# Optimization experiments

Measured on AMD Instinct MI355X. Metric: run time of the kernel, lower is better.

## Reference

```python
import jax, jax.numpy as jnp
import numpy as np

D = 2048   # input_dim == output_dim (original scatter-adds into zeros_like(x))
E = 16     # num_experts
K = 2      # expert_top_k
B = 2048   # tokens


def setup_inputs() -> dict:
    key = jax.random.key(0)
    ks = jax.random.split(key, 6)
    s = 0.02
    return {
        "x":  jax.random.normal(ks[0], (B, D), jnp.float32),
        "W1": (jax.random.normal(ks[1], (E, D, D), jnp.float32) * s),
        "b1": jnp.zeros((E, D), jnp.float32),
        "W2": (jax.random.normal(ks[2], (E, D, D), jnp.float32) * s),
        "b2": jnp.zeros((E, D), jnp.float32),
        "Wg": (jax.random.normal(ks[3], (D, E), jnp.float32) * s),
        "bg": jnp.zeros((E,), jnp.float32),
    }


def reference(x, W1, b1, W2, b2, Wg, bg):
    # --- gating ---
    gate_scores = x @ Wg + bg                                  # (B, E)
    topk_scores, topk_idx = jax.lax.top_k(gate_scores, K)      # (B, K)
    gate_act = jax.nn.softmax(topk_scores, axis=-1)            # (B, K) softmax over top-k only
    onehot = jax.nn.one_hot(topk_idx, E, dtype=x.dtype)        # (B, K, E)
    combine = jnp.einsum('bk,bke->be', gate_act, onehot)       # (B, E) gate weight per expert (0 if unrouted)
    routing_mask = onehot.sum(axis=1)                          # (B, E) in {0,1}

    # --- expert MLPs (dense grouped form; unrouted tokens zeroed by combine) ---
    h = jax.nn.relu(jnp.einsum('bd,edh->ebh', x, W1) + b1[:, None, :])   # (E, B, D)
    y = jnp.einsum('ebh,eho->ebo', h, W2) + b2[:, None, :]               # (E, B, D)
    out = jnp.einsum('ebo,be->bo', y, combine)                           # (B, D) weighted scatter-add combine

    # --- aux losses (torch.var is unbiased, ddof=1) ---
    loads = routing_mask.sum(axis=0)                            # tokens per expert
    load_loss = jnp.var(loads, ddof=1) / (E * (B / E))          # balance_factor = num_experts * expected_load = B
    imp = jax.nn.softmax(gate_scores, axis=-1).sum(axis=0)      # (E,)
    importance_loss = jnp.var(imp, ddof=1) / (imp.mean() + 1e-8)
    return out, load_loss, importance_loss
```

## Files before the change

### kernel.cpp

```cpp
#include <hip/hip_runtime.h>
#include <hip/hip_bf16.h>
#include <stdint.h>

#define DIM   2048
#define NEXP  16
#define TOPK  2
#define NTOK  2048
#define NSLOT (NTOK*TOPK)

typedef __bf16 bf16_t;
typedef __attribute__((ext_vector_type(4))) __bf16 bf16x4;
typedef __attribute__((ext_vector_type(8))) __bf16 bf16x8;
typedef __attribute__((ext_vector_type(4))) float f32x4;

#define WS_CURSOR    0
#define WS_COUNTS    1024
#define WS_OFFS      1152
#define WS_TOK_TOP   4096
#define WS_TOK_GATE  20480
#define WS_SLOT_TOK  36864
#define WS_SLOT_GATE 53248
#define WS_IMPP      69632
#define WS_XBF       262144
#define WS_H         (WS_XBF + NTOK*DIM*2)

__global__ __launch_bounds__(256) void k_convert_x(const float* __restrict__ x,
                                                   bf16_t* __restrict__ xb) {
    int i = (blockIdx.x * 256 + threadIdx.x) * 4;
    float4 v = *reinterpret_cast<const float4*>(x + i);
    bf16x4 o;
    o[0] = (bf16_t)v.x; o[1] = (bf16_t)v.y; o[2] = (bf16_t)v.z; o[3] = (bf16_t)v.w;
    *reinterpret_cast<bf16x4*>(xb + i) = o;
}

__global__ __launch_bounds__(256) void k_gate(const float* __restrict__ x,
                                              const float* __restrict__ Wg,
                                              const float* __restrict__ bg,
                                              float* __restrict__ imp_partial,
                                              int* __restrict__ tok_top,
                                              float* __restrict__ tok_gate) {
    const int tok  = blockIdx.x * 4 + (threadIdx.x >> 6);
    const int lane = threadIdx.x & 63;
    const float* xr = x + (size_t)tok * DIM;

    float acc[NEXP];
#pragma unroll
    for (int e = 0; e < NEXP; e++) acc[e] = 0.f;

#pragma unroll
    for (int i = 0; i < 8; i++) {
        int d = (i * 64 + lane) * 4;
        float4 xv = *reinterpret_cast<const float4*>(xr + d);
        const float4* wr = reinterpret_cast<const float4*>(Wg + (size_t)d * NEXP);
#pragma unroll
        for (int c = 0; c < 4; c++) {
            float xc = (&xv.x)[c];
#pragma unroll
            for (int j = 0; j < 4; j++) {
                float4 w = wr[c * 4 + j];
                acc[j * 4 + 0] += xc * w.x;
                acc[j * 4 + 1] += xc * w.y;
                acc[j * 4 + 2] += xc * w.z;
                acc[j * 4 + 3] += xc * w.w;
            }
        }
    }
#pragma unroll
    for (int e = 0; e < NEXP; e++) {
#pragma unroll
        for (int off = 32; off > 0; off >>= 1) acc[e] += __shfl_xor(acc[e], off, 64);
    }

    if (lane == 0) {
        float sc[NEXP];
#pragma unroll
        for (int e = 0; e < NEXP; e++) sc[e] = acc[e] + bg[e];
        float mx = sc[0];
#pragma unroll
        for (int e = 1; e < NEXP; e++) mx = fmaxf(mx, sc[e]);
        float p[NEXP], sum = 0.f;
#pragma unroll
        for (int e = 0; e < NEXP; e++) { p[e] = expf(sc[e] - mx); sum += p[e]; }
        float inv = 1.f / sum;
#pragma unroll
        for (int e = 0; e < NEXP; e++) imp_partial[tok * NEXP + e] = p[e] * inv;
        int i0 = 0;
#pragma unroll
        for (int e = 1; e < NEXP; e++) if (sc[e] > sc[i0]) i0 = e;
        int i1 = -1;
#pragma unroll
        for (int e = 0; e < NEXP; e++)
            if (e != i0 && (i1 < 0 || sc[e] > sc[i1])) i1 = e;
        float g0 = 1.f / (1.f + expf(sc[i1] - sc[i0]));
        tok_top[tok * 2 + 0] = i0; tok_top[tok * 2 + 1] = i1;
        tok_gate[tok * 2 + 0] = g0; tok_gate[tok * 2 + 1] = 1.f - g0;
    }
}

__global__ __launch_bounds__(256) void k_finalize(const float* __restrict__ imp_partial,
                                                  const int* __restrict__ tok_top,
                                                  int* __restrict__ counts,
                                                  int* __restrict__ offs,
                                                  float* __restrict__ losses) {
    __shared__ int   scnt[NEXP];
    __shared__ float ired[16][NEXP + 1];
    const int t = threadIdx.x;
    if (t < NEXP) scnt[t] = 0;
    __syncthreads();
    for (int i = t; i < NSLOT; i += 256) atomicAdd(&scnt[tok_top[i]], 1);
    {
        const int e = t & 15, ch = t >> 4;
        float s = 0.f;
        for (int r = ch * 128; r < ch * 128 + 128; r++) s += imp_partial[r * NEXP + e];
        ired[ch][e] = s;
    }
    __syncthreads();
    if (t == 0) {
        int o = 0;
        float cntf[NEXP];
        for (int e = 0; e < NEXP; e++) {
            counts[e] = scnt[e]; offs[e] = o; o += scnt[e]; cntf[e] = (float)scnt[e];
        }
        offs[NEXP] = o;
        float m = (float)o / NEXP, v = 0.f;
        for (int e = 0; e < NEXP; e++) { float d = cntf[e] - m; v += d * d; }
        losses[0] = (v / (NEXP - 1)) / (float)NTOK;
        float imp[NEXP];
        for (int e = 0; e < NEXP; e++) {
            float s = 0.f;
            for (int ch = 0; ch < 16; ch++) s += ired[ch][e];
            imp[e] = s;
        }
        float ms = 0.f;
        for (int e = 0; e < NEXP; e++) ms += imp[e];
        ms /= NEXP;
        float vv = 0.f;
        for (int e = 0; e < NEXP; e++) { float d = imp[e] - ms; vv += d * d; }
        losses[1] = (vv / (NEXP - 1)) / (ms + 1e-8f);
    }
}

__global__ __launch_bounds__(256) void k_scatter(const int* __restrict__ tok_top,
                                                 const float* __restrict__ tok_gate,
                                                 const int* __restrict__ offs,
                                                 int* __restrict__ cursor,
                                                 int* __restrict__ slot_tok,
                                                 float* __restrict__ slot_gate) {
    int i = blockIdx.x * 256 + threadIdx.x;
    int e = tok_top[i];
    int pos = atomicAdd(&cursor[e * 16], 1);
    int slot = offs[e] + pos;
    slot_tok[slot] = i >> 1;
    slot_gate[slot] = tok_gate[i];
}

#define BM 256
#define BN 128
#define BK 32
#define APITCH 32
#define BPITCH 40

template <int PHASE>
__global__ __launch_bounds__(512) void k_gemm(const float* __restrict__ Wall,
                                              const float* __restrict__ bias,
                                              const bf16_t* __restrict__ Asrc,
                                              const int* __restrict__ counts,
                                              const int* __restrict__ offs,
                                              const int* __restrict__ slot_tok,
                                              const float* __restrict__ slot_gate,
                                              bf16_t* __restrict__ Hout,
                                              float* __restrict__ out) {
    const int e  = blockIdx.z;
    const int n0 = blockIdx.x * BN;
    const int m0 = blockIdx.y * BM;
    const int cnt = counts[e];
    if (m0 >= cnt) return;
    const int off = offs[e];

    __shared__ bf16_t As[BM * APITCH];
    __shared__ bf16_t Bs[BN * BPITCH];

    const int t = threadIdx.x;
    const int lane = t & 63, wv = t >> 6;
    const int wm = wv & 3, wn = wv >> 2;
    const int l15 = lane & 15, q = lane >> 4;

    const bf16_t* arow[2];
#pragma unroll
    for (int i = 0; i < 2; i++) {
        int rl = wv * 32 + i * 16 + (lane >> 2);
        int slot = off + m0 + rl;
        slot = slot < (NSLOT - 1) ? slot : (NSLOT - 1);
        int srow = (PHASE == 1) ? slot_tok[slot] : slot;
        arow[i] = Asrc + (size_t)srow * DIM + (lane & 3) * 8;
    }
    const int bn = t & 127, kh = t >> 7;
    const float* bsrc = Wall + (size_t)e * DIM * DIM + (size_t)(kh * 8) * DIM + n0 + bn;
    bf16_t* bdst = &Bs[bn * BPITCH + kh * 8];

    f32x4 acc[4][4] = {};

    for (int k0 = 0; k0 < DIM; k0 += BK) {
        __syncthreads();
#pragma unroll
        for (int i = 0; i < 2; i++) {
            bf16_t* ldst = &As[(wv * 32 + i * 16) * APITCH];
            __builtin_amdgcn_global_load_lds(
                (const __attribute__((address_space(1))) uint32_t*)(arow[i] + k0),
                (__attribute__((address_space(3))) uint32_t*)ldst, 16, 0, 0);
        }
        {
            const float* bs = bsrc + (size_t)k0 * DIM;
            float v[8];
#pragma unroll
            for (int kk = 0; kk < 8; kk++) v[kk] = bs[(size_t)kk * DIM];
            bf16x8 pk;
#pragma unroll
            for (int kk = 0; kk < 8; kk++) pk[kk] = (bf16_t)v[kk];
            *reinterpret_cast<bf16x8*>(bdst) = pk;
        }
        __syncthreads();

        bf16x8 af[4], bfr[4];
#pragma unroll
        for (int mf = 0; mf < 4; mf++)
            af[mf] = *reinterpret_cast<const bf16x8*>(&As[(wm * 64 + mf * 16 + l15) * APITCH + q * 8]);
#pragma unroll
        for (int nf = 0; nf < 4; nf++)
            bfr[nf] = *reinterpret_cast<const bf16x8*>(&Bs[(wn * 64 + nf * 16 + l15) * BPITCH + q * 8]);
#pragma unroll
        for (int mf = 0; mf < 4; mf++)
#pragma unroll
            for (int nf = 0; nf < 4; nf++)
                acc[mf][nf] = __builtin_amdgcn_mfma_f32_16x16x32_bf16(af[mf], bfr[nf], acc[mf][nf], 0, 0, 0);
    }

    const int rows_here = cnt - m0;
#pragma unroll
    for (int mf = 0; mf < 4; mf++) {
#pragma unroll
        for (int r = 0; r < 4; r++) {
            int rl = wm * 64 + mf * 16 + q * 4 + r;
            if (rl >= rows_here) continue;
            int slot = off + m0 + rl;
            if (PHASE == 1) {
#pragma unroll
                for (int nf = 0; nf < 4; nf++) {
                    int col = n0 + wn * 64 + nf * 16 + l15;
                    float h = acc[mf][nf][r] + bias[e * DIM + col];
                    h = fmaxf(h, 0.f);
                    Hout[(size_t)slot * DIM + col] = (bf16_t)h;
                }
            } else {
                float g = slot_gate[slot];
                int tok = slot_tok[slot];
#pragma unroll
                for (int nf = 0; nf < 4; nf++) {
                    int col = n0 + wn * 64 + nf * 16 + l15;
                    float y = acc[mf][nf][r] + bias[e * DIM + col];
                    atomicAdd(&out[(size_t)tok * DIM + col], g * y);
                }
            }
        }
    }
}

extern "C" void kernel_launch(void* const* d_in, const int* in_sizes, int n_in,
                              void* d_out, int out_size, void* d_ws, size_t ws_size,
                              hipStream_t stream) {
    const float* x  = (const float*)d_in[0];
    const float* W1 = (const float*)d_in[1];
    const float* b1 = (const float*)d_in[2];
    const float* W2 = (const float*)d_in[3];
    const float* b2 = (const float*)d_in[4];
    const float* Wg = (const float*)d_in[5];
    const float* bg = (const float*)d_in[6];
    float* out = (float*)d_out;
    char*  ws  = (char*)d_ws;

    int*    cursor    = (int*)(ws + WS_CURSOR);
    int*    counts    = (int*)(ws + WS_COUNTS);
    int*    offs      = (int*)(ws + WS_OFFS);
    int*    tok_top   = (int*)(ws + WS_TOK_TOP);
    float*  tok_gate  = (float*)(ws + WS_TOK_GATE);
    int*    slot_tok  = (int*)(ws + WS_SLOT_TOK);
    float*  slot_gate = (float*)(ws + WS_SLOT_GATE);
    float*  imp_part  = (float*)(ws + WS_IMPP);
    bf16_t* xbf       = (bf16_t*)(ws + WS_XBF);
    bf16_t* H         = (bf16_t*)(ws + WS_H);

    hipMemsetAsync(cursor, 0, 1024, stream);
    hipMemsetAsync(out, 0, (size_t)NTOK * DIM * sizeof(float), stream);

    k_convert_x<<<NTOK * DIM / 1024, 256, 0, stream>>>(x, xbf);
    k_gate<<<NTOK / 4, 256, 0, stream>>>(x, Wg, bg, imp_part, tok_top, tok_gate);
    k_finalize<<<1, 256, 0, stream>>>(imp_part, tok_top, counts, offs, out + (size_t)NTOK * DIM);
    k_scatter<<<NSLOT / 256, 256, 0, stream>>>(tok_top, tok_gate, offs, cursor, slot_tok, slot_gate);

    dim3 grid(DIM / BN, NTOK / BM, NEXP);
    k_gemm<1><<<grid, 512, 0, stream>>>(W1, b1, xbf, counts, offs, slot_tok, slot_gate, H, nullptr);
    k_gemm<2><<<grid, 512, 0, stream>>>(W2, b2, H, counts, offs, slot_tok, slot_gate, nullptr, out);
}
```

Measured before the change: 932.2 us.

## Fuse preprocessing kernels and double-buffer the grouped expert GEMM with smaller N tiles

The x-to-bf16 conversion is folded into the gating kernel, and the slot scatter is folded into the single-block finalize kernel using shared-memory cursors. This removes two kernel launches and a memset. The expert GEMM gets double-buffered LDS so the next K-step's global loads overlap the current step's MFMAs, an XOR swizzle on A reads, BN reduced from 128 to 64, and an occupancy hint in launch bounds. Halving BN doubles the block count and the redundant A-tile reads, and it makes each block re-read the W tile per M block in a different pattern.

```diff
diff --git a/kernel.cpp b/kernel.cpp
--- a/kernel.cpp
+++ b/kernel.cpp
@@ -13,7 +13,6 @@
 typedef __attribute__((ext_vector_type(8))) __bf16 bf16x8;
 typedef __attribute__((ext_vector_type(4))) float f32x4;
 
-#define WS_CURSOR    0
 #define WS_COUNTS    1024
 #define WS_OFFS      1152
 #define WS_TOK_TOP   4096
@@ -24,24 +23,17 @@
 #define WS_XBF       262144
 #define WS_H         (WS_XBF + NTOK*DIM*2)
 
-__global__ __launch_bounds__(256) void k_convert_x(const float* __restrict__ x,
-                                                   bf16_t* __restrict__ xb) {
-    int i = (blockIdx.x * 256 + threadIdx.x) * 4;
-    float4 v = *reinterpret_cast<const float4*>(x + i);
-    bf16x4 o;
-    o[0] = (bf16_t)v.x; o[1] = (bf16_t)v.y; o[2] = (bf16_t)v.z; o[3] = (bf16_t)v.w;
-    *reinterpret_cast<bf16x4*>(xb + i) = o;
-}
-
 __global__ __launch_bounds__(256) void k_gate(const float* __restrict__ x,
                                               const float* __restrict__ Wg,
                                               const float* __restrict__ bg,
                                               float* __restrict__ imp_partial,
                                               int* __restrict__ tok_top,
-                                              float* __restrict__ tok_gate) {
+                                              float* __restrict__ tok_gate,
+                                              bf16_t* __restrict__ xb) {
     const int tok  = blockIdx.x * 4 + (threadIdx.x >> 6);
     const int lane = threadIdx.x & 63;
     const float* xr = x + (size_t)tok * DIM;
+    bf16_t* xbr = xb + (size_t)tok * DIM;
 
     float acc[NEXP];
 #pragma unroll
@@ -51,6 +43,9 @@
     for (int i = 0; i < 8; i++) {
         int d = (i * 64 + lane) * 4;
         float4 xv = *reinterpret_cast<const float4*>(xr + d);
+        bf16x4 o;
+        o[0] = (bf16_t)xv.x; o[1] = (bf16_t)xv.y; o[2] = (bf16_t)xv.z; o[3] = (bf16_t)xv.w;
+        *reinterpret_cast<bf16x4*>(xbr + d) = o;
         const float4* wr = reinterpret_cast<const float4*>(Wg + (size_t)d * NEXP);
 #pragma unroll
         for (int c = 0; c < 4; c++) {
@@ -99,13 +94,18 @@
 
 __global__ __launch_bounds__(256) void k_finalize(const float* __restrict__ imp_partial,
                                                   const int* __restrict__ tok_top,
+                                                  const float* __restrict__ tok_gate,
                                                   int* __restrict__ counts,
                                                   int* __restrict__ offs,
+                                                  int* __restrict__ slot_tok,
+                                                  float* __restrict__ slot_gate,
                                                   float* __restrict__ losses) {
     __shared__ int   scnt[NEXP];
+    __shared__ int   soff[NEXP];
+    __shared__ int   scur[NEXP];
     __shared__ float ired[16][NEXP + 1];
     const int t = threadIdx.x;
-    if (t < NEXP) scnt[t] = 0;
+    if (t < NEXP) { scnt[t] = 0; scur[t] = 0; }
     __syncthreads();
     for (int i = t; i < NSLOT; i += 256) atomicAdd(&scnt[tok_top[i]], 1);
     {
@@ -119,7 +119,7 @@
         int o = 0;
         float cntf[NEXP];
         for (int e = 0; e < NEXP; e++) {
-            counts[e] = scnt[e]; offs[e] = o; o += scnt[e]; cntf[e] = (float)scnt[e];
+            counts[e] = scnt[e]; soff[e] = o; offs[e] = o; o += scnt[e]; cntf[e] = (float)scnt[e];
         }
         offs[NEXP] = o;
         float m = (float)o / NEXP, v = 0.f;
@@ -138,38 +138,33 @@
         for (int e = 0; e < NEXP; e++) { float d = imp[e] - ms; vv += d * d; }
         losses[1] = (vv / (NEXP - 1)) / (ms + 1e-8f);
     }
+    __syncthreads();
+    for (int i = t; i < NSLOT; i += 256) {
+        int e = tok_top[i];
+        int pos = atomicAdd(&scur[e], 1);
+        int slot = soff[e] + pos;
+        slot_tok[slot] = i >> 1;
+        slot_gate[slot] = tok_gate[i];
+    }
 }
 
-__global__ __launch_bounds__(256) void k_scatter(const int* __restrict__ tok_top,
-                                                 const float* __restrict__ tok_gate,
-                                                 const int* __restrict__ offs,
-                                                 int* __restrict__ cursor,
-                                                 int* __restrict__ slot_tok,
-                                                 float* __restrict__ slot_gate) {
-    int i = blockIdx.x * 256 + threadIdx.x;
-    int e = tok_top[i];
-    int pos = atomicAdd(&cursor[e * 16], 1);
-    int slot = offs[e] + pos;
-    slot_tok[slot] = i >> 1;
-    slot_gate[slot] = tok_gate[i];
-}
-
 #define BM 256
-#define BN 128
+#define BN 64
 #define BK 32
+#define NSTEPS (DIM/BK)
 #define APITCH 32
 #define BPITCH 40
 
 template <int PHASE>
-__global__ __launch_bounds__(512) void k_gemm(const float* __restrict__ Wall,
-                                              const float* __restrict__ bias,
-                                              const bf16_t* __restrict__ Asrc,
-                                              const int* __restrict__ counts,
-                                              const int* __restrict__ offs,
-                                              const int* __restrict__ slot_tok,
-                                              const float* __restrict__ slot_gate,
-                                              bf16_t* __restrict__ Hout,
-                                              float* __restrict__ out) {
+__global__ __launch_bounds__(512, 6) void k_gemm(const float* __restrict__ Wall,
+                                                 const float* __restrict__ bias,
+                                                 const bf16_t* __restrict__ Asrc,
+                                                 const int* __restrict__ counts,
+                                                 const int* __restrict__ offs,
+                                                 const int* __restrict__ slot_tok,
+                                                 const float* __restrict__ slot_gate,
+                                                 bf16_t* __restrict__ Hout,
+                                                 float* __restrict__ out) {
     const int e  = blockIdx.z;
     const int n0 = blockIdx.x * BN;
     const int m0 = blockIdx.y * BM;
@@ -177,11 +172,11 @@
     if (m0 >= cnt) return;
     const int off = offs[e];
 
-    __shared__ bf16_t As[BM * APITCH];
-    __shared__ bf16_t Bs[BN * BPITCH];
-
-    const int t = threadIdx.x;
-    const int lane = t & 63, wv = t >> 6;
+    __shared__ bf16_t As[2][BM * APITCH];
+    __shared__ bf16_t Bs[2][BN * BPITCH];
+
+    const int tid  = threadIdx.x;
+    const int lane = tid & 63, wv = tid >> 6;
     const int wm = wv & 3, wn = wv >> 2;
     const int l15 = lane & 15, q = lane >> 4;
 
@@ -192,47 +187,72 @@
         int slot = off + m0 + rl;
         slot = slot < (NSLOT - 1) ? slot : (NSLOT - 1);
         int srow = (PHASE == 1) ? slot_tok[slot] : slot;
-        arow[i] = Asrc + (size_t)srow * DIM + (lane & 3) * 8;
-    }
-    const int bn = t & 127, kh = t >> 7;
-    const float* bsrc = Wall + (size_t)e * DIM * DIM + (size_t)(kh * 8) * DIM + n0 + bn;
-    bf16_t* bdst = &Bs[bn * BPITCH + kh * 8];
-
-    f32x4 acc[4][4] = {};
-
-    for (int k0 = 0; k0 < DIM; k0 += BK) {
+        int gchunk = (lane & 3) ^ ((lane >> 3) & 3);
+        arow[i] = Asrc + (size_t)srow * DIM + gchunk * 8;
+    }
+    const int bn = tid & 63, kh = tid >> 6;
+    const float* bsrc = Wall + (size_t)e * DIM * DIM + (size_t)(kh * 4) * DIM + n0 + bn;
+    bf16_t* bdst0 = &Bs[0][bn * BPITCH + kh * 4];
+    bf16_t* bdst1 = &Bs[1][bn * BPITCH + kh * 4];
+
+    f32x4 acc[4][2] = {};
+    float bv[4];
+
+#pragma unroll
+    for (int i = 0; i < 2; i++) {
+        bf16_t* ldst = &As[0][(wv * 32 + i * 16) * APITCH];
+        __builtin_amdgcn_global_load_lds(
+            (const __attribute__((address_space(1))) uint32_t*)(arow[i]),
+            (__attribute__((address_space(3))) uint32_t*)ldst, 16, 0, 0);
+    }
+#pragma unroll
+    for (int kk = 0; kk < 4; kk++) bv[kk] = bsrc[(size_t)kk * DIM];
+    {
+        bf16x4 pk;
+#pragma unroll
+        for (int kk = 0; kk < 4; kk++) pk[kk] = (bf16_t)bv[kk];
+        *reinterpret_cast<bf16x4*>(bdst0) = pk;
+    }
+    __syncthreads();
+
+    const int akey = (l15 >> 1) & 3;
+
+    for (int t = 0; t < NSTEPS; t++) {
+        const int cur = t & 1;
+        const int k1 = (t + 1) * BK;
+        if (t + 1 < NSTEPS) {
+#pragma unroll
+            for (int i = 0; i < 2; i++) {
+                bf16_t* ldst = &As[cur ^ 1][(wv * 32 + i * 16) * APITCH];
+                __builtin_amdgcn_global_load_lds(
+                    (const __attribute__((address_space(1))) uint32_t*)(arow[i] + k1),
+                    (__attribute__((address_space(3))) uint32_t*)ldst, 16, 0, 0);
+            }
+            const float* bs = bsrc + (size_t)k1 * DIM;
+#pragma unroll
+            for (int kk = 0; kk < 4; kk++) bv[kk] = bs[(size_t)kk * DIM];
+        }
+        bf16x8 af[4], bfr[2];
+#pragma unroll
+        for (int mf = 0; mf < 4; mf++)
+            af[mf] = *reinterpret_cast<const bf16x8*>(
+                &As[cur][(wm * 64 + mf * 16 + l15) * APITCH + ((q ^ akey) * 8)]);
+#pragma unroll
+        for (int nf = 0; nf < 2; nf++)
+            bfr[nf] = *reinterpret_cast<const bf16x8*>(
+                &Bs[cur][(wn * 32 + nf * 16 + l15) * BPITCH + q * 8]);
+#pragma unroll
+        for (int mf = 0; mf < 4; mf++)
+#pragma unroll
+            for (int nf = 0; nf < 2; nf++)
+                acc[mf][nf] = __builtin_amdgcn_mfma_f32_16x16x32_bf16(af[mf], bfr[nf], acc[mf][nf], 0, 0, 0);
+        if (t + 1 < NSTEPS) {
+            bf16x4 pk;
+#pragma unroll
+            for (int kk = 0; kk < 4; kk++) pk[kk] = (bf16_t)bv[kk];
+            *reinterpret_cast<bf16x4*>((cur ^ 1) ? bdst1 : bdst0) = pk;
+        }
         __syncthreads();
-#pragma unroll
-        for (int i = 0; i < 2; i++) {
-            bf16_t* ldst = &As[(wv * 32 + i * 16) * APITCH];
-            __builtin_amdgcn_global_load_lds(
-                (const __attribute__((address_space(1))) uint32_t*)(arow[i] + k0),
-                (__attribute__((address_space(3))) uint32_t*)ldst, 16, 0, 0);
-        }
-        {
-            const float* bs = bsrc + (size_t)k0 * DIM;
-            float v[8];
-#pragma unroll
-            for (int kk = 0; kk < 8; kk++) v[kk] = bs[(size_t)kk * DIM];
-            bf16x8 pk;
-#pragma unroll
-            for (int kk = 0; kk < 8; kk++) pk[kk] = (bf16_t)v[kk];
-            *reinterpret_cast<bf16x8*>(bdst) = pk;
-        }
-        __syncthreads();
-
-        bf16x8 af[4], bfr[4];
-#pragma unroll
-        for (int mf = 0; mf < 4; mf++)
-            af[mf] = *reinterpret_cast<const bf16x8*>(&As[(wm * 64 + mf * 16 + l15) * APITCH + q * 8]);
-#pragma unroll
-        for (int nf = 0; nf < 4; nf++)
-            bfr[nf] = *reinterpret_cast<const bf16x8*>(&Bs[(wn * 64 + nf * 16 + l15) * BPITCH + q * 8]);
-#pragma unroll
-        for (int mf = 0; mf < 4; mf++)
-#pragma unroll
-            for (int nf = 0; nf < 4; nf++)
-                acc[mf][nf] = __builtin_amdgcn_mfma_f32_16x16x32_bf16(af[mf], bfr[nf], acc[mf][nf], 0, 0, 0);
     }
 
     const int rows_here = cnt - m0;
@@ -245,8 +265,8 @@
             int slot = off + m0 + rl;
             if (PHASE == 1) {
 #pragma unroll
-                for (int nf = 0; nf < 4; nf++) {
-                    int col = n0 + wn * 64 + nf * 16 + l15;
+                for (int nf = 0; nf < 2; nf++) {
+                    int col = n0 + wn * 32 + nf * 16 + l15;
                     float h = acc[mf][nf][r] + bias[e * DIM + col];
                     h = fmaxf(h, 0.f);
                     Hout[(size_t)slot * DIM + col] = (bf16_t)h;
@@ -255,8 +275,8 @@
                 float g = slot_gate[slot];
                 int tok = slot_tok[slot];
 #pragma unroll
-                for (int nf = 0; nf < 4; nf++) {
-                    int col = n0 + wn * 64 + nf * 16 + l15;
+                for (int nf = 0; nf < 2; nf++) {
+                    int col = n0 + wn * 32 + nf * 16 + l15;
                     float y = acc[mf][nf][r] + bias[e * DIM + col];
                     atomicAdd(&out[(size_t)tok * DIM + col], g * y);
                 }
@@ -278,7 +298,6 @@
     float* out = (float*)d_out;
     char*  ws  = (char*)d_ws;
 
-    int*    cursor    = (int*)(ws + WS_CURSOR);
     int*    counts    = (int*)(ws + WS_COUNTS);
     int*    offs      = (int*)(ws + WS_OFFS);
     int*    tok_top   = (int*)(ws + WS_TOK_TOP);
@@ -289,13 +308,11 @@
     bf16_t* xbf       = (bf16_t*)(ws + WS_XBF);
     bf16_t* H         = (bf16_t*)(ws + WS_H);
 
-    hipMemsetAsync(cursor, 0, 1024, stream);
     hipMemsetAsync(out, 0, (size_t)NTOK * DIM * sizeof(float), stream);
 
-    k_convert_x<<<NTOK * DIM / 1024, 256, 0, stream>>>(x, xbf);
-    k_gate<<<NTOK / 4, 256, 0, stream>>>(x, Wg, bg, imp_part, tok_top, tok_gate);
-    k_finalize<<<1, 256, 0, stream>>>(imp_part, tok_top, counts, offs, out + (size_t)NTOK * DIM);
-    k_scatter<<<NSLOT / 256, 256, 0, stream>>>(tok_top, tok_gate, offs, cursor, slot_tok, slot_gate);
+    k_gate<<<NTOK / 4, 256, 0, stream>>>(x, Wg, bg, imp_part, tok_top, tok_gate, xbf);
+    k_finalize<<<1, 256, 0, stream>>>(imp_part, tok_top, tok_gate, counts, offs,
+                                      slot_tok, slot_gate, out + (size_t)NTOK * DIM);
 
     dim3 grid(DIM / BN, NTOK / BM, NEXP);
     k_gemm<1><<<grid, 512, 0, stream>>>(W1, b1, xbf, counts, offs, slot_tok, slot_gate, H, nullptr);
```

After: 877.7 us. 5.8% less time.
